# Kernel optimization log

Measured on AMD Instinct MI355X. Metric: run time of the kernel, lower is better.

Reference implementation:

```python
import jax, jax.numpy as jnp
import numpy as np

NUM_USERS = 100000
NUM_ITEMS = 50000
LATENT_DIM = 64
N_LAYERS = 3
N_EDGES = 6_400_000
QUERY_BATCH = 1024


def setup_inputs() -> dict:
    key = jax.random.key(0)
    k1, k2, k3, k4, k5, k6 = jax.random.split(key, 6)
    # nn.init.normal_(std=0.1) on both embedding tables
    user_emb = jax.random.normal(k1, (NUM_USERS, LATENT_DIM), jnp.float32) * 0.1
    item_emb = jax.random.normal(k2, (NUM_ITEMS, LATENT_DIM), jnp.float32) * 0.1
    # sparse normalized adjacency in COO form over N = users + items nodes
    N = NUM_USERS + NUM_ITEMS
    edge_src = jax.random.randint(k3, (N_EDGES,), 0, N, dtype=jnp.int32)
    edge_dst = jax.random.randint(k4, (N_EDGES,), 0, N, dtype=jnp.int32)
    # positive normalization weights (stand-in for D^-1/2 A D^-1/2 values)
    edge_val = jax.random.uniform(k5, (N_EDGES,), jnp.float32)
    users = jax.random.randint(k6, (QUERY_BATCH,), 0, NUM_USERS, dtype=jnp.int32)
    return {
        "user_emb": user_emb,
        "item_emb": item_emb,
        "edge_val": edge_val,
        "edge_src": edge_src,
        "edge_dst": edge_dst,
        "users": users,
    }


def _computer(user_emb, item_emb, edge_val, edge_src, edge_dst):
    # LightGCN.computer(): n_layers of SpMM propagation + layer mean-pooling
    N = NUM_USERS + NUM_ITEMS
    all_emb = jnp.concatenate([user_emb, item_emb], axis=0)  # [N, d]
    acc = all_emb
    x = all_emb
    for _ in range(N_LAYERS):
        # torch.sparse.mm(G, x): gather rows by src, scale by edge value, scatter-add to dst
        x = jax.ops.segment_sum(edge_val[:, None] * x[edge_src], edge_dst,
                                num_segments=N)
        acc = acc + x
    light_out = acc / jnp.asarray(N_LAYERS + 1, dtype=acc.dtype)
    return light_out[:NUM_USERS], light_out[NUM_USERS:]


def reference(user_emb, item_emb, edge_val, edge_src, edge_dst, users):
    all_users, all_items = _computer(user_emb, item_emb, edge_val, edge_src, edge_dst)
    users_emb = all_users[users]  # [B, d]
    # getUsersRating: sigmoid(U @ I^T) over all items -> [B, n_items]
    rating = jax.nn.sigmoid(users_emb @ all_items.T)
    return rating
```

## Files before the change

kernel.cpp:

```cpp
#include <hip/hip_runtime.h>
#include <hip/hip_fp16.h>

#define NUSERS 100000
#define NITEMS 50000
#define NN (NUSERS + NITEMS)
#define D 64
#define NE 6400000
#define QB 1024
#define PSZ 256
#define NP ((NN + PSZ - 1) / PSZ)
#define NBLKB 256
#define EPB (NE / NBLKB)
#define CNTN (NP * NBLKB)
#define PB_CHUNK 4096

__global__ __launch_bounds__(256) void countB_kernel(const int* __restrict__ dst,
                                                     int* __restrict__ counts) {
    __shared__ int hist[NP];
    const int t = threadIdx.x, b = blockIdx.x;
    for (int j = t; j < NP; j += 256) hist[j] = 0;
    __syncthreads();
    const int e0 = b * EPB, e1 = e0 + EPB;
    for (int i = e0 + t; i < e1; i += 256)
        atomicAdd(&hist[dst[i] >> 8], 1);
    __syncthreads();
    for (int j = t; j < NP; j += 256)
        counts[j * NBLKB + b] = hist[j];
}

__global__ __launch_bounds__(1024) void scan_kernel(const int* __restrict__ cnt,
                                                    int* __restrict__ out, int nn) {
    __shared__ int wsum[16];
    __shared__ int s_carry, s_tot;
    const int t = threadIdx.x;
    const int lane = t & 63;
    const int wid = t >> 6;
    if (t == 0) s_carry = 0;
    __syncthreads();
    const int CH = 16384;
    for (int chunk = 0; chunk < nn; chunk += CH) {
        const int i0 = chunk + t * 16;
        int c[16];
        if (i0 + 16 <= nn) {
#pragma unroll
            for (int q = 0; q < 4; ++q) {
                int4 v = *reinterpret_cast<const int4*>(cnt + i0 + q * 4);
                c[q * 4 + 0] = v.x; c[q * 4 + 1] = v.y;
                c[q * 4 + 2] = v.z; c[q * 4 + 3] = v.w;
            }
        } else {
#pragma unroll
            for (int q = 0; q < 16; ++q) c[q] = (i0 + q < nn) ? cnt[i0 + q] : 0;
        }
        int v = 0;
#pragma unroll
        for (int q = 0; q < 16; ++q) v += c[q];
        int s = v;
#pragma unroll
        for (int off = 1; off < 64; off <<= 1) {
            int y = __shfl_up(s, off, 64);
            if (lane >= off) s += y;
        }
        if (lane == 63) wsum[wid] = s;
        __syncthreads();
        if (t < 16) {
            int w = wsum[t];
            int ss = w;
#pragma unroll
            for (int off = 1; off < 16; off <<= 1) {
                int y = __shfl_up(ss, off, 16);
                if (t >= off) ss += y;
            }
            wsum[t] = ss - w;
            if (t == 15) s_tot = ss;
        }
        __syncthreads();
        int run = s_carry + wsum[wid] + (s - v);
        int o[16];
#pragma unroll
        for (int q = 0; q < 16; ++q) { o[q] = run; run += c[q]; }
        if (i0 + 16 <= nn) {
#pragma unroll
            for (int q = 0; q < 4; ++q)
                *reinterpret_cast<int4*>(out + i0 + q * 4) =
                    make_int4(o[q * 4], o[q * 4 + 1], o[q * 4 + 2], o[q * 4 + 3]);
        } else {
#pragma unroll
            for (int q = 0; q < 16; ++q) if (i0 + q < nn) out[i0 + q] = o[q];
        }
        __syncthreads();
        if (t == 0) s_carry += s_tot;
        __syncthreads();
    }
    if (t == 0) out[nn] = s_carry;
}

__global__ __launch_bounds__(1024) void placeB_kernel(const int* __restrict__ src,
                                                      const int* __restrict__ dst,
                                                      const float* __restrict__ val,
                                                      const int* __restrict__ offs,
                                                      int2* __restrict__ tmp) {
    __shared__ int  cur[NP];
    __shared__ int  chist[NP];
    __shared__ int  cbase[NP];
    __shared__ int2 stage[PB_CHUNK];
    __shared__ int  gpos[PB_CHUNK];
    const int t = threadIdx.x, b = blockIdx.x;
    for (int p = t; p < NP; p += 1024) cur[p] = offs[p * NBLKB + b];
    const int e0 = b * EPB, e1 = e0 + EPB;
    for (int c0 = e0; c0 < e1; c0 += PB_CHUNK) {
        const int csize = min(PB_CHUNK, e1 - c0);
        for (int p = t; p < NP; p += 1024) chist[p] = 0;
        __syncthreads();
        int  ep[4], eslot[4];
        int2 epay[4];
#pragma unroll
        for (int q = 0; q < 4; ++q) {
            int i = c0 + t + q * 1024;
            ep[q] = -1;
            if (i < e1) {
                int d = dst[i];
                int p = d >> 8;
                ep[q] = p;
                epay[q] = make_int2(src[i] | ((d & (PSZ - 1)) << 18),
                                    __float_as_int(val[i]));
                eslot[q] = atomicAdd(&chist[p], 1);
            }
        }
        __syncthreads();
        if (t < 64) {
            const int per = (NP + 63) / 64;
            int base = t * per;
            int loc[(NP + 63) / 64];
            int run = 0;
#pragma unroll
            for (int q = 0; q < (NP + 63) / 64; ++q) {
                int idx = base + q;
                int c = (idx < NP) ? chist[idx] : 0;
                loc[q] = run; run += c;
            }
            int s = run;
#pragma unroll
            for (int off = 1; off < 64; off <<= 1) {
                int y = __shfl_up(s, off, 64);
                if (t >= off) s += y;
            }
            int excl = s - run;
#pragma unroll
            for (int q = 0; q < (NP + 63) / 64; ++q) {
                int idx = base + q;
                if (idx < NP) cbase[idx] = excl + loc[q];
            }
        }
        __syncthreads();
#pragma unroll
        for (int q = 0; q < 4; ++q) {
            if (ep[q] >= 0) {
                int s = cbase[ep[q]] + eslot[q];
                stage[s] = epay[q];
                gpos[s]  = cur[ep[q]] + eslot[q];
            }
        }
        __syncthreads();
        for (int k = t; k < csize; k += 1024)
            tmp[gpos[k]] = stage[k];
        for (int p = t; p < NP; p += 1024) cur[p] += chist[p];
        __syncthreads();
    }
}

__global__ __launch_bounds__(1024) void phaseC_kernel(const int2* __restrict__ tmp,
                                                      const int* __restrict__ offs,
                                                      int* __restrict__ row_start,
                                                      int2* __restrict__ csr) {
    __shared__ int hist[PSZ];
    __shared__ int cur[PSZ];
    __shared__ int wsum[4];
    const int p = blockIdx.x;
    const int t = threadIdx.x;
    const int lane = t & 63, wid = t >> 6;
    const int node0 = p * PSZ;
    const int nloc = min(PSZ, NN - node0);
    const int rb = offs[p * NBLKB];
    const int re = (p == NP - 1) ? NE : offs[(p + 1) * NBLKB];
    if (t < PSZ) hist[t] = 0;
    __syncthreads();
    for (int i = rb + t; i < re; i += 1024)
        atomicAdd(&hist[tmp[i].x >> 18], 1);
    __syncthreads();
    int v = 0, s = 0;
    if (t < PSZ) {
        v = hist[t];
        s = v;
#pragma unroll
        for (int off = 1; off < 64; off <<= 1) {
            int y = __shfl_up(s, off, 64);
            if (lane >= off) s += y;
        }
        if (lane == 63) wsum[wid] = s;
    }
    __syncthreads();
    if (t == 0) {
        int a = wsum[0], b2 = wsum[1], c = wsum[2];
        wsum[1] = a; wsum[2] = a + b2; wsum[3] = a + b2 + c; wsum[0] = 0;
    }
    __syncthreads();
    if (t < PSZ) {
        int base = rb + wsum[wid] + (s - v);
        cur[t] = base;
        if (t < nloc) row_start[node0 + t] = base;
    }
    if (p == 0 && t == 0) row_start[NN] = NE;
    __syncthreads();
    for (int i = rb + t; i < re; i += 1024) {
        int2 e = tmp[i];
        int dl = e.x >> 18;
        int pos = atomicAdd(&cur[dl], 1);
        csr[pos] = make_int2(e.x & 0x3FFFF, e.y);
    }
}

__global__ __launch_bounds__(256) void conv0_kernel(const float4* __restrict__ ue4,
                                                    const float4* __restrict__ ie4,
                                                    ushort4* __restrict__ x0) {
    const int U4 = NUSERS * (D / 4);
    const int T4 = NN * (D / 4);
    int i = blockIdx.x * 256 + threadIdx.x;
    if (i >= T4) return;
    float4 v = (i < U4) ? ue4[i] : ie4[i - U4];
    x0[i] = make_ushort4(__half_as_ushort(__float2half_rn(v.x)),
                         __half_as_ushort(__float2half_rn(v.y)),
                         __half_as_ushort(__float2half_rn(v.z)),
                         __half_as_ushort(__float2half_rn(v.w)));
}

#define GATHER_LOOP_H(XH)                                                      \
    {                                                                          \
        int i = b;                                                             \
        for (; i + 8 <= e; i += 8) {                                           \
            int2 E[8];                                                         \
            _Pragma("unroll")                                                  \
            for (int q = 0; q < 8; ++q) E[q] = csr[i + q];                     \
            float r[8];                                                        \
            _Pragma("unroll")                                                  \
            for (int q = 0; q < 8; ++q)                                        \
                r[q] = __half2float(XH[(size_t)E[q].x * D + lane]);            \
            _Pragma("unroll")                                                  \
            for (int q = 0; q < 8; ++q)                                        \
                a = fmaf(__int_as_float(E[q].y), r[q], a);                     \
        }                                                                      \
        for (; i < e; ++i) {                                                   \
            int2 e0 = csr[i];                                                  \
            a = fmaf(__int_as_float(e0.y),                                     \
                     __half2float(XH[(size_t)e0.x * D + lane]), a);            \
        }                                                                      \
    }

template <int M>
__global__ __launch_bounds__(256) void spmm_kernel(const __half* __restrict__ xh,
                                                   const float* __restrict__ ie,
                                                   __half* __restrict__ xout,
                                                   float* __restrict__ acc_items,
                                                   const int* __restrict__ row_start,
                                                   const int2* __restrict__ csr) {
    int wave = (blockIdx.x << 2) | (threadIdx.x >> 6);
    int row = __builtin_amdgcn_readfirstlane(wave);
    if (row >= NN) return;
    const int lane = threadIdx.x & 63;
    int b = __builtin_amdgcn_readfirstlane(row_start[row]);
    int e = __builtin_amdgcn_readfirstlane(row_start[row + 1]);
    float a = 0.f;
    GATHER_LOOP_H(xh)
    xout[(size_t)row * D + lane] = __float2half_rn(a);
    if (row >= NUSERS) {
        size_t o = (size_t)(row - NUSERS) * D + lane;
        if (M == 0)
            acc_items[o] = ie[o] + a;
        else
            acc_items[o] += a;
    }
}

__global__ __launch_bounds__(256) void spmm_items_kernel(const __half* __restrict__ x2h,
                                                         const float* __restrict__ acc_items,
                                                         const int* __restrict__ row_start,
                                                         const int2* __restrict__ csr,
                                                         float* __restrict__ items_s) {
    int wave = (blockIdx.x << 2) | (threadIdx.x >> 6);
    int it = __builtin_amdgcn_readfirstlane(wave);
    if (it >= NITEMS) return;
    const int row = NUSERS + it;
    const int lane = threadIdx.x & 63;
    int b = __builtin_amdgcn_readfirstlane(row_start[row]);
    int e = __builtin_amdgcn_readfirstlane(row_start[row + 1]);
    float a = 0.f;
    GATHER_LOOP_H(x2h)
    size_t o = (size_t)it * D + lane;
    items_s[o] = acc_items[o] + a;
}

__global__ __launch_bounds__(256) void user_final_kernel(const float* __restrict__ ue,
                                                         const __half* __restrict__ x1h,
                                                         const __half* __restrict__ x2h,
                                                         const int* __restrict__ users,
                                                         const int* __restrict__ row_start,
                                                         const int2* __restrict__ csr,
                                                         float* __restrict__ ug) {
    int w = (blockIdx.x << 2) | (threadIdx.x >> 6);
    if (w >= QB) return;
    const int lane = threadIdx.x & 63;
    int row = __builtin_amdgcn_readfirstlane(users[w]);
    int b = __builtin_amdgcn_readfirstlane(row_start[row]);
    int e = __builtin_amdgcn_readfirstlane(row_start[row + 1]);
    float a = 0.f;
    GATHER_LOOP_H(x2h)
    size_t o = (size_t)row * D + lane;
    const float sc = 1.0f / 16.0f;
    ug[(size_t)w * D + lane] =
        (ue[o] + __half2float(x1h[o]) + __half2float(x2h[o]) + a) * sc;
}

__global__ __launch_bounds__(256) void rating_kernel(const float* __restrict__ items_s,
                                                     const float* __restrict__ ug,
                                                     float* __restrict__ out) {
    const int i = blockIdx.x * 256 + threadIdx.x;
    const bool valid = i < NITEMS;
    const int ic = valid ? i : 0;
    float4 ir[16];
    const float4* irow = reinterpret_cast<const float4*>(items_s) + (size_t)ic * (D / 4);
#pragma unroll
    for (int k = 0; k < 16; ++k) ir[k] = irow[k];
    const float4* ug4 = reinterpret_cast<const float4*>(ug);
    const int u0 = blockIdx.y * 128;
    for (int g = 0; g < 16; ++g) {
        const int ub = u0 + g * 8;
        float s[8];
#pragma unroll
        for (int j = 0; j < 8; ++j) s[j] = 0.f;
#pragma unroll
        for (int k = 0; k < 16; ++k) {
            const float4 iv = ir[k];
#pragma unroll
            for (int j = 0; j < 8; ++j) {
                const float4 uv = ug4[(ub + j) * (D / 4) + k];
                s[j] = fmaf(iv.x, uv.x, s[j]);
                s[j] = fmaf(iv.y, uv.y, s[j]);
                s[j] = fmaf(iv.z, uv.z, s[j]);
                s[j] = fmaf(iv.w, uv.w, s[j]);
            }
        }
        if (valid) {
#pragma unroll
            for (int j = 0; j < 8; ++j) {
                float r = 1.0f / (1.0f + __expf(-s[j]));
                out[(size_t)(ub + j) * NITEMS + i] = r;
            }
        }
    }
}

extern "C" void kernel_launch(void* const* d_in, const int* in_sizes, int n_in,
                              void* d_out, int out_size, void* d_ws, size_t ws_size,
                              hipStream_t stream) {
    const float* user_emb = (const float*)d_in[0];
    const float* item_emb = (const float*)d_in[1];
    const float* edge_val = (const float*)d_in[2];
    const int*   edge_src = (const int*)d_in[3];
    const int*   edge_dst = (const int*)d_in[4];
    const int*   users    = (const int*)d_in[5];

    float*  ob  = (float*)d_out;
    int2*   csr = (int2*)ob;
    int2*   tmp = csr + NE;
    __half* x0h = (__half*)(tmp + NE);
    __half* x1h = x0h + (size_t)NN * D;
    __half* x2h = x1h + (size_t)NN * D;
    float*  acc = (float*)(x2h + (size_t)NN * D);
    int*    row_start = (int*)(acc + (size_t)NITEMS * D);
    int*    counts    = row_start + 150080;
    int*    offs      = counts + CNTN;

    float* items_s = (float*)d_ws;
    float* ug      = items_s + (size_t)NITEMS * D;

    countB_kernel<<<NBLKB, 256, 0, stream>>>(edge_dst, counts);
    scan_kernel<<<1, 1024, 0, stream>>>(counts, offs, CNTN);
    placeB_kernel<<<NBLKB, 1024, 0, stream>>>(edge_src, edge_dst, edge_val, offs, tmp);
    phaseC_kernel<<<NP, 1024, 0, stream>>>(tmp, offs, row_start, csr);

    conv0_kernel<<<(NN * (D / 4) + 255) / 256, 256, 0, stream>>>(
        (const float4*)user_emb, (const float4*)item_emb, (ushort4*)x0h);

    spmm_kernel<0><<<37500, 256, 0, stream>>>(x0h, item_emb, x1h, acc, row_start, csr);
    spmm_kernel<1><<<37500, 256, 0, stream>>>(x1h, nullptr, x2h, acc, row_start, csr);
    spmm_items_kernel<<<12500, 256, 0, stream>>>(x2h, acc, row_start, csr, items_s);
    user_final_kernel<<<QB / 4, 256, 0, stream>>>(user_emb, x1h, x2h, users,
                                                  row_start, csr, ug);

    rating_kernel<<<dim3((NITEMS + 255) / 256, QB / 128), 256, 0, stream>>>(items_s, ug, (float*)d_out);
}
```

Before: 627.8 us.

## Stage user tile in LDS and accumulate 64 users per thread in rating kernel

The rating GEMM kernel now loads a 64-user tile of the gathered user embeddings into shared memory once per block. Each thread streams its item row one float4 at a time and keeps 64 accumulators, instead of holding the item row in registers and reading user rows from global memory in groups of 8. Output sigmoid values are written with nontemporal stores to limit cache pollution from the 200MB output. The change raises the register count (64 accumulators) and doubles the grid's y dimension, which can lower occupancy.

Measured after the change: 647.7 us. +3.2%, slower.

```diff
diff --git a/kernel.cpp b/kernel.cpp
--- a/kernel.cpp
+++ b/kernel.cpp
@@ -13,6 +13,7 @@
 #define EPB (NE / NBLKB)
 #define CNTN (NP * NBLKB)
 #define PB_CHUNK 4096
+#define UPB 64
 
 __global__ __launch_bounds__(256) void countB_kernel(const int* __restrict__ dst,
                                                      int* __restrict__ counts) {
@@ -323,38 +324,38 @@
 __global__ __launch_bounds__(256) void rating_kernel(const float* __restrict__ items_s,
                                                      const float* __restrict__ ug,
                                                      float* __restrict__ out) {
-    const int i = blockIdx.x * 256 + threadIdx.x;
-    const bool valid = i < NITEMS;
-    const int ic = valid ? i : 0;
-    float4 ir[16];
-    const float4* irow = reinterpret_cast<const float4*>(items_s) + (size_t)ic * (D / 4);
-#pragma unroll
-    for (int k = 0; k < 16; ++k) ir[k] = irow[k];
+    __shared__ float4 uls[UPB][16];
+    const int t = threadIdx.x;
+    const int u0 = blockIdx.y * UPB;
     const float4* ug4 = reinterpret_cast<const float4*>(ug);
-    const int u0 = blockIdx.y * 128;
-    for (int g = 0; g < 16; ++g) {
-        const int ub = u0 + g * 8;
-        float s[8];
-#pragma unroll
-        for (int j = 0; j < 8; ++j) s[j] = 0.f;
-#pragma unroll
-        for (int k = 0; k < 16; ++k) {
-            const float4 iv = ir[k];
-#pragma unroll
-            for (int j = 0; j < 8; ++j) {
-                const float4 uv = ug4[(ub + j) * (D / 4) + k];
-                s[j] = fmaf(iv.x, uv.x, s[j]);
-                s[j] = fmaf(iv.y, uv.y, s[j]);
-                s[j] = fmaf(iv.z, uv.z, s[j]);
-                s[j] = fmaf(iv.w, uv.w, s[j]);
-            }
-        }
-        if (valid) {
-#pragma unroll
-            for (int j = 0; j < 8; ++j) {
-                float r = 1.0f / (1.0f + __expf(-s[j]));
-                out[(size_t)(ub + j) * NITEMS + i] = r;
-            }
+    for (int q = t; q < UPB * 16; q += 256)
+        (&uls[0][0])[q] = ug4[u0 * 16 + q];
+    __syncthreads();
+
+    const int i = blockIdx.x * 256 + t;
+    const int ic = (i < NITEMS) ? i : (NITEMS - 1);
+    const float4* irow = reinterpret_cast<const float4*>(items_s) + (size_t)ic * 16;
+
+    float acc[UPB];
+#pragma unroll
+    for (int j = 0; j < UPB; ++j) acc[j] = 0.f;
+
+    for (int k = 0; k < 16; ++k) {
+        const float4 ir = irow[k];
+#pragma unroll
+        for (int j = 0; j < UPB; ++j) {
+            const float4 uv = uls[j][k];
+            acc[j] = fmaf(ir.x, uv.x, acc[j]);
+            acc[j] = fmaf(ir.y, uv.y, acc[j]);
+            acc[j] = fmaf(ir.z, uv.z, acc[j]);
+            acc[j] = fmaf(ir.w, uv.w, acc[j]);
+        }
+    }
+    if (i < NITEMS) {
+#pragma unroll
+        for (int j = 0; j < UPB; ++j) {
+            float r = 1.0f / (1.0f + __expf(-acc[j]));
+            __builtin_nontemporal_store(r, &out[(size_t)(u0 + j) * NITEMS + i]);
         }
     }
 }
@@ -397,5 +398,5 @@
     user_final_kernel<<<QB / 4, 256, 0, stream>>>(user_emb, x1h, x2h, users,
                                                   row_start, csr, ug);
 
-    rating_kernel<<<dim3((NITEMS + 255) / 256, QB / 128), 256, 0, stream>>>(items_s, ug, (float*)d_out);
-}
+    rating_kernel<<<dim3((NITEMS + 255) / 256, QB / UPB), 256, 0, stream>>>(items_s, ug, (float*)d_out);
+}
```

## Compute rating GEMM with fp16 MFMA and nontemporal output stores

Applied to the files above, without the earlier changes.

Stores the final item and query-user embeddings in fp16 and replaces the scalar fp32 dot-product rating kernel with a wave-level MFMA 16x16x32 f16 kernel. Each wave computes a 16-user by 64-item tile, applies sigmoid, and writes it with nontemporal stores. This aims to cut the ALU cost of the dense 1024x50000x64 product and reduce cache pollution from the large output write. It gives up precision in the final embeddings and scores, because inputs are rounded to fp16.

Result: faster. 549.1 us (-12.5%).

```diff
diff --git a/kernel.cpp b/kernel.cpp
--- a/kernel.cpp
+++ b/kernel.cpp
@@ -13,6 +13,10 @@
 #define EPB (NE / NBLKB)
 #define CNTN (NP * NBLKB)
 #define PB_CHUNK 4096
+#define RIT ((NITEMS + 63) / 64)
+
+typedef _Float16 half8 __attribute__((ext_vector_type(8)));
+typedef float f32x4 __attribute__((ext_vector_type(4)));
 
 __global__ __launch_bounds__(256) void countB_kernel(const int* __restrict__ dst,
                                                      int* __restrict__ counts) {
@@ -285,7 +289,7 @@
                                                          const float* __restrict__ acc_items,
                                                          const int* __restrict__ row_start,
                                                          const int2* __restrict__ csr,
-                                                         float* __restrict__ items_s) {
+                                                         _Float16* __restrict__ items_h) {
     int wave = (blockIdx.x << 2) | (threadIdx.x >> 6);
     int it = __builtin_amdgcn_readfirstlane(wave);
     if (it >= NITEMS) return;
@@ -296,7 +300,7 @@
     float a = 0.f;
     GATHER_LOOP_H(x2h)
     size_t o = (size_t)it * D + lane;
-    items_s[o] = acc_items[o] + a;
+    items_h[o] = (_Float16)(acc_items[o] + a);
 }
 
 __global__ __launch_bounds__(256) void user_final_kernel(const float* __restrict__ ue,
@@ -305,7 +309,7 @@
                                                          const int* __restrict__ users,
                                                          const int* __restrict__ row_start,
                                                          const int2* __restrict__ csr,
-                                                         float* __restrict__ ug) {
+                                                         _Float16* __restrict__ ug_h) {
     int w = (blockIdx.x << 2) | (threadIdx.x >> 6);
     if (w >= QB) return;
     const int lane = threadIdx.x & 63;
@@ -316,44 +320,48 @@
     GATHER_LOOP_H(x2h)
     size_t o = (size_t)row * D + lane;
     const float sc = 1.0f / 16.0f;
-    ug[(size_t)w * D + lane] =
-        (ue[o] + __half2float(x1h[o]) + __half2float(x2h[o]) + a) * sc;
-}
-
-__global__ __launch_bounds__(256) void rating_kernel(const float* __restrict__ items_s,
-                                                     const float* __restrict__ ug,
+    ug_h[(size_t)w * D + lane] =
+        (_Float16)((ue[o] + __half2float(x1h[o]) + __half2float(x2h[o]) + a) * sc);
+}
+
+__global__ __launch_bounds__(256) void rating_kernel(const _Float16* __restrict__ items_h,
+                                                     const _Float16* __restrict__ ug_h,
                                                      float* __restrict__ out) {
-    const int i = blockIdx.x * 256 + threadIdx.x;
-    const bool valid = i < NITEMS;
-    const int ic = valid ? i : 0;
-    float4 ir[16];
-    const float4* irow = reinterpret_cast<const float4*>(items_s) + (size_t)ic * (D / 4);
-#pragma unroll
-    for (int k = 0; k < 16; ++k) ir[k] = irow[k];
-    const float4* ug4 = reinterpret_cast<const float4*>(ug);
-    const int u0 = blockIdx.y * 128;
-    for (int g = 0; g < 16; ++g) {
-        const int ub = u0 + g * 8;
-        float s[8];
-#pragma unroll
-        for (int j = 0; j < 8; ++j) s[j] = 0.f;
-#pragma unroll
-        for (int k = 0; k < 16; ++k) {
-            const float4 iv = ir[k];
-#pragma unroll
-            for (int j = 0; j < 8; ++j) {
-                const float4 uv = ug4[(ub + j) * (D / 4) + k];
-                s[j] = fmaf(iv.x, uv.x, s[j]);
-                s[j] = fmaf(iv.y, uv.y, s[j]);
-                s[j] = fmaf(iv.z, uv.z, s[j]);
-                s[j] = fmaf(iv.w, uv.w, s[j]);
-            }
-        }
-        if (valid) {
-#pragma unroll
-            for (int j = 0; j < 8; ++j) {
-                float r = 1.0f / (1.0f + __expf(-s[j]));
-                out[(size_t)(ub + j) * NITEMS + i] = r;
+    const int lane = threadIdx.x & 63;
+    const int w = threadIdx.x >> 6;
+    const int u0 = blockIdx.y * 64 + w * 16;
+    const int i0 = blockIdx.x * 64;
+    const int lr  = lane & 15;
+    const int kb8 = (lane >> 4) * 8;
+
+    const int urow = u0 + lr;
+    const half8 a0 = *reinterpret_cast<const half8*>(ug_h + urow * D + kb8);
+    const half8 a1 = *reinterpret_cast<const half8*>(ug_h + urow * D + 32 + kb8);
+
+    f32x4 acc[4];
+    half8 b0[4], b1[4];
+#pragma unroll
+    for (int sub = 0; sub < 4; ++sub) {
+        int irow = i0 + sub * 16 + lr;
+        irow = (irow < NITEMS) ? irow : (NITEMS - 1);
+        b0[sub] = *reinterpret_cast<const half8*>(items_h + (size_t)irow * D + kb8);
+        b1[sub] = *reinterpret_cast<const half8*>(items_h + (size_t)irow * D + 32 + kb8);
+        acc[sub] = {0.f, 0.f, 0.f, 0.f};
+    }
+#pragma unroll
+    for (int sub = 0; sub < 4; ++sub) {
+        acc[sub] = __builtin_amdgcn_mfma_f32_16x16x32_f16(a0, b0[sub], acc[sub], 0, 0, 0);
+        acc[sub] = __builtin_amdgcn_mfma_f32_16x16x32_f16(a1, b1[sub], acc[sub], 0, 0, 0);
+    }
+    const int ubase = u0 + (lane >> 4) * 4;
+#pragma unroll
+    for (int sub = 0; sub < 4; ++sub) {
+        const int item = i0 + sub * 16 + lr;
+        if (item < NITEMS) {
+#pragma unroll
+            for (int r = 0; r < 4; ++r) {
+                float sg = 1.0f / (1.0f + __expf(-acc[sub][r]));
+                __builtin_nontemporal_store(sg, &out[(size_t)(ubase + r) * NITEMS + item]);
             }
         }
     }
@@ -380,8 +388,8 @@
     int*    counts    = row_start + 150080;
     int*    offs      = counts + CNTN;
 
-    float* items_s = (float*)d_ws;
-    float* ug      = items_s + (size_t)NITEMS * D;
+    _Float16* items_h = (_Float16*)d_ws;
+    _Float16* ug_h    = items_h + (size_t)NITEMS * D;
 
     countB_kernel<<<NBLKB, 256, 0, stream>>>(edge_dst, counts);
     scan_kernel<<<1, 1024, 0, stream>>>(counts, offs, CNTN);
@@ -393,9 +401,9 @@
 
     spmm_kernel<0><<<37500, 256, 0, stream>>>(x0h, item_emb, x1h, acc, row_start, csr);
     spmm_kernel<1><<<37500, 256, 0, stream>>>(x1h, nullptr, x2h, acc, row_start, csr);
-    spmm_items_kernel<<<12500, 256, 0, stream>>>(x2h, acc, row_start, csr, items_s);
+    spmm_items_kernel<<<12500, 256, 0, stream>>>(x2h, acc, row_start, csr, items_h);
     user_final_kernel<<<QB / 4, 256, 0, stream>>>(user_emb, x1h, x2h, users,
-                                                  row_start, csr, ug);
-
-    rating_kernel<<<dim3((NITEMS + 255) / 256, QB / 128), 256, 0, stream>>>(items_s, ug, (float*)d_out);
-}
+                                                  row_start, csr, ug_h);
+
+    rating_kernel<<<dim3(RIT, QB / 64), 256, 0, stream>>>(items_h, ug_h, (float*)d_out);
+}
```
